# Kernel optimization log

Measured on AMD Instinct MI355X. Metric: run time of the kernel, lower is better.

Reference implementation:

```python
import jax, jax.numpy as jnp
import numpy as np

B, S = 1024, 256
E, EU = 8, 1            # total experts, universal experts
ES = E - EU             # specialized experts
UW = 0.3                # universal_expert_weight
NSTEPS = 1001
COV = 512
H = 128
DATA_DIM = 2


def setup_inputs() -> dict:
    key = jax.random.key(0)
    ks = iter(jax.random.split(key, 64))

    def nrm(shape, s=0.02):
        return jax.random.normal(next(ks), shape, jnp.float32) * s

    inp = {
        "y_t": jax.random.normal(next(ks), (B, S, 1), jnp.float32),
        "y_0_hat": jax.random.normal(next(ks), (B, S, 1), jnp.float32),
        "cov_embedding": jax.random.normal(next(ks), (B, COV), jnp.float32),
        "t": jax.random.randint(next(ks), (B,), 0, NSTEPS),
    }
    for l, nin in zip((1, 2, 3), (DATA_DIM, H, H)):
        inp[f"l{l}_emb"] = jax.random.uniform(next(ks), (NSTEPS, H), jnp.float32)  # embed.weight.uniform_()
        inp[f"l{l}_W"] = nrm((E, nin, H))      # per-expert Linear weights
        inp[f"l{l}_b"] = jnp.zeros((E, H), jnp.float32)
        inp[f"l{l}_Wc"] = nrm((COV, H))        # cov_projection
        inp[f"l{l}_bc"] = jnp.zeros((H,), jnp.float32)
        inp[f"l{l}_Wr1"] = nrm((COV, COV // 2))  # specialized_router layer 1
        inp[f"l{l}_br1"] = jnp.zeros((COV // 2,), jnp.float32)
        inp[f"l{l}_Wr2"] = nrm((COV // 2, ES))   # specialized_router layer 2
        inp[f"l{l}_br2"] = jnp.zeros((ES,), jnp.float32)
    inp["W4"] = nrm((H, 1))
    inp["b4"] = jnp.zeros((1,), jnp.float32)
    return inp


def _moe_layer(x, t, cov, emb, W, b, Wc, bc, Wr1, br1, Wr2, br2):
    # x: [B,S,in]; t: [B] int; cov: [B,COV]
    gamma = emb[t][:, None, :]                                   # [B,1,H]
    hr = jax.nn.relu(cov @ Wr1 + br1)                            # router (dropout inactive in eval)
    rw = jax.nn.softmax(hr @ Wr2 + br2, axis=-1) * (1.0 - UW)    # [B,ES] specialized routing weights
    w = jnp.concatenate(
        [jnp.full((x.shape[0], EU), UW / EU, x.dtype), rw], axis=1
    )                                                            # [B,E] full routing weights
    # gamma factors out of the weighted sum over experts, so fuse expert GEMMs + weighting:
    mix = jnp.einsum('bsi,eio,be->bso', x, W, w) + jnp.einsum('be,eo->bo', w, b)[:, None, :]
    mix = gamma * mix
    cov_gamma = cov @ Wc + bc                                    # [B,H]
    mix = mix * (1.0 + cov_gamma[:, None, :])
    usage = rw.mean(axis=0)                                      # mean over batch
    load = jnp.mean((usage - 1.0 / ES) ** 2)                     # mse vs uniform
    return mix, load


def reference(y_t, y_0_hat, cov_embedding, t,
              l1_emb, l1_W, l1_b, l1_Wc, l1_bc, l1_Wr1, l1_br1, l1_Wr2, l1_br2,
              l2_emb, l2_W, l2_b, l2_Wc, l2_bc, l2_Wr1, l2_br1, l2_Wr2, l2_br2,
              l3_emb, l3_W, l3_b, l3_Wc, l3_bc, l3_Wr1, l3_br1, l3_Wr2, l3_br2,
              W4, b4):
    h = jnp.concatenate([y_t, y_0_hat], axis=-1)                 # cat_y_pred: [B,S,2]
    h, ld1 = _moe_layer(h, t, cov_embedding, l1_emb, l1_W, l1_b, l1_Wc, l1_bc, l1_Wr1, l1_br1, l1_Wr2, l1_br2)
    h = jax.nn.softplus(h)
    h, ld2 = _moe_layer(h, t, cov_embedding, l2_emb, l2_W, l2_b, l2_Wc, l2_bc, l2_Wr1, l2_br1, l2_Wr2, l2_br2)
    h = jax.nn.softplus(h)
    h, ld3 = _moe_layer(h, t, cov_embedding, l3_emb, l3_W, l3_b, l3_Wc, l3_bc, l3_Wr1, l3_br1, l3_Wr2, l3_br2)
    h = jax.nn.softplus(h)
    out = h @ W4 + b4                                            # [B,S,1] velocity
    return out, ld1 + ld2 + ld3
```

## Files before the change

### kernel.cpp

```cpp
#include <hip/hip_runtime.h>
#include <hip/hip_bf16.h>
#include <math.h>

#define B_    1024
#define S_    256
#define COV_  512
#define H_    128
#define E_    8
#define ES_   7

#define W_WS_OFF   0
#define COVG_OFF   24576
#define USAGE_OFF  417792

#define AT_STRIDE  136
#define WT_STRIDE  40

typedef __attribute__((ext_vector_type(8))) short bf16x8;
typedef __attribute__((ext_vector_type(4))) float f32x4;

__device__ __forceinline__ float softplus_f(float x) {
    return fmaxf(x, 0.0f) + __logf(1.0f + __expf(-fabsf(x)));
}

__device__ __forceinline__ unsigned pk2_bf16(float a, float b) {
    __hip_bfloat162 h = __float22bfloat162_rn(make_float2(a, b));
    return *reinterpret_cast<unsigned*>(&h);
}
__device__ __forceinline__ void split_pair(float a, float b, unsigned &hi, unsigned &lo) {
    hi = pk2_bf16(a, b);
    float ha = __uint_as_float(hi << 16);
    float hb = __uint_as_float(hi & 0xffff0000u);
    lo = pk2_bf16(a - ha, b - hb);
}

struct RouterArgs {
    const float* cov;
    const float* Wr1[3];
    const float* br1[3];
    const float* Wr2[3];
    const float* br2[3];
    const float* Wc[3];
    const float* bc[3];
    float* ws;
};

__global__ __launch_bounds__(384) void router_kernel(RouterArgs a) {
    const int l   = blockIdx.y;
    const int b0  = blockIdx.x * 4;
    const int tid = threadIdx.x;

    __shared__ float hr[4][256];
    __shared__ float susage[ES_];
    if (tid < ES_) susage[tid] = 0.0f;

    const float* __restrict__ c0 = a.cov + (size_t)(b0 + 0) * COV_;
    const float* __restrict__ c1 = a.cov + (size_t)(b0 + 1) * COV_;
    const float* __restrict__ c2 = a.cov + (size_t)(b0 + 2) * COV_;
    const float* __restrict__ c3 = a.cov + (size_t)(b0 + 3) * COV_;

    {
        const float* __restrict__ Wp;
        int stride; float bias;
        if (tid < 256) { Wp = a.Wr1[l] + tid;         stride = 256; bias = a.br1[l][tid]; }
        else           { Wp = a.Wc[l]  + (tid - 256); stride = 128; bias = a.bc[l][tid - 256]; }

        float acc0 = 0.f, acc1 = 0.f, acc2 = 0.f, acc3 = 0.f;
        #pragma unroll 8
        for (int k = 0; k < COV_; ++k) {
            const float wv = Wp[(size_t)k * stride];
            acc0 = fmaf(c0[k], wv, acc0);
            acc1 = fmaf(c1[k], wv, acc1);
            acc2 = fmaf(c2[k], wv, acc2);
            acc3 = fmaf(c3[k], wv, acc3);
        }
        if (tid < 256) {
            hr[0][tid] = fmaxf(acc0 + bias, 0.0f);
            hr[1][tid] = fmaxf(acc1 + bias, 0.0f);
            hr[2][tid] = fmaxf(acc2 + bias, 0.0f);
            hr[3][tid] = fmaxf(acc3 + bias, 0.0f);
        } else {
            const int j = tid - 256;
            a.ws[COVG_OFF + (size_t)(l * B_ + b0 + 0) * H_ + j] = acc0 + bias;
            a.ws[COVG_OFF + (size_t)(l * B_ + b0 + 1) * H_ + j] = acc1 + bias;
            a.ws[COVG_OFF + (size_t)(l * B_ + b0 + 2) * H_ + j] = acc2 + bias;
            a.ws[COVG_OFF + (size_t)(l * B_ + b0 + 3) * H_ + j] = acc3 + bias;
        }
    }
    __syncthreads();

    {
        const int wave = tid >> 6;
        const int lane = tid & 63;
        if (wave < 4) {
            const int bb = wave;
            const int o = lane >> 3;
            const int g = lane & 7;
            float p = 0.0f;
            if (o < ES_) {
                #pragma unroll
                for (int m = 0; m < 32; ++m) {
                    const int k = g * 32 + m;
                    p = fmaf(hr[bb][k], a.Wr2[l][k * ES_ + o], p);
                }
            }
            p += __shfl_xor(p, 1);
            p += __shfl_xor(p, 2);
            p += __shfl_xor(p, 4);
            const float lg = p + ((o < ES_) ? a.br2[l][o] : 0.0f);
            float v[ES_];
            #pragma unroll
            for (int oo = 0; oo < ES_; ++oo) v[oo] = __shfl(lg, oo * 8, 64);
            if (lane == 0) {
                const int b = b0 + bb;
                float mx = v[0];
                #pragma unroll
                for (int oo = 1; oo < ES_; ++oo) mx = fmaxf(mx, v[oo]);
                float ex[ES_]; float s = 0.0f;
                #pragma unroll
                for (int oo = 0; oo < ES_; ++oo) { ex[oo] = __expf(v[oo] - mx); s += ex[oo]; }
                const float inv = 0.7f / s;
                float* wout = a.ws + W_WS_OFF + (size_t)(l * B_ + b) * 8;
                wout[0] = 0.3f;
                #pragma unroll
                for (int oo = 0; oo < ES_; ++oo) {
                    const float rwv = ex[oo] * inv;
                    wout[1 + oo] = rwv;
                    atomicAdd(&susage[oo], rwv);
                }
            }
        }
    }
    __syncthreads();
    if (tid < ES_) atomicAdd(a.ws + USAGE_OFF + l * ES_ + tid, susage[tid]);
}

struct MainArgs {
    const float* y_t;
    const float* y0;
    const int*   t;
    const float* emb[3];
    const float* W1;
    const float* W2;
    const float* W3;
    const float* b_[3];
    const float* W4;
    const float* b4;
    float* ws;
    float* out;
};

__global__ __launch_bounds__(1024, 4) void main_kernel(MainArgs a) {
    __shared__ unsigned short Ahi[256 * AT_STRIDE];
    __shared__ unsigned short Alo[256 * AT_STRIDE];
    __shared__ unsigned short WtBuf[2][128 * WT_STRIDE];
    __shared__ float GPs[2][128];
    __shared__ float GPBs[2][128];
    __shared__ float W4s[128];

    const int tid  = threadIdx.x;
    const int b    = blockIdx.x;
    const int lane = tid & 63;
    const int w    = tid >> 6;
    const int wm   = w >> 1;
    const int wn   = w & 1;
    const int nl   = lane & 15;
    const int quad = lane >> 4;
    const int tb   = a.t[b];

    float* L1f = (float*)WtBuf;

    if (tid < 384) {
        const int l = tid >> 7, j = tid & 127;
        const float* wv = a.ws + W_WS_OFF + (size_t)(l * B_ + b) * 8;
        const float gamma = a.emb[l][tb * H_ + j];
        const float covg  = a.ws[COVG_OFF + (size_t)(l * B_ + b) * H_ + j];
        const float gp = gamma * (1.0f + covg);
        const float* bl = a.b_[l];
        float bm = 0.0f;
        #pragma unroll
        for (int e = 0; e < E_; ++e) bm = fmaf(wv[e], bl[e * H_ + j], bm);
        if (l == 0) {
            float s0 = 0.0f, s1 = 0.0f;
            #pragma unroll
            for (int e = 0; e < E_; ++e) {
                s0 = fmaf(wv[e], a.W1[e * 256 + j], s0);
                s1 = fmaf(wv[e], a.W1[e * 256 + 128 + j], s1);
            }
            L1f[j]       = gp * s0;
            L1f[128 + j] = gp * s1;
            L1f[256 + j] = gp * bm;
        } else {
            GPs[l - 1][j]  = gp;
            GPBs[l - 1][j] = gp * bm;
        }
    }
    if (tid < 128) W4s[tid] = a.W4[tid];
    __syncthreads();

    {
        const int tok = tid >> 2;
        const int jh  = (tid & 3) * 32;
        const float x0 = a.y_t[b * S_ + tok];
        const float x1 = a.y0[b * S_ + tok];
        #pragma unroll
        for (int g = 0; g < 4; ++g) {
            const int jb = jh + g * 8;
            unsigned hp[4], lp[4];
            #pragma unroll
            for (int p = 0; p < 4; ++p) {
                const int j0 = jb + 2 * p;
                float m0 = fmaf(x0, L1f[j0],     fmaf(x1, L1f[128 + j0],     L1f[256 + j0]));
                float m1 = fmaf(x0, L1f[j0 + 1], fmaf(x1, L1f[128 + j0 + 1], L1f[256 + j0 + 1]));
                split_pair(softplus_f(m0), softplus_f(m1), hp[p], lp[p]);
            }
            *(uint4*)&Ahi[tok * AT_STRIDE + jb] = make_uint4(hp[0], hp[1], hp[2], hp[3]);
            *(uint4*)&Alo[tok * AT_STRIDE + jb] = make_uint4(lp[0], lp[1], lp[2], lp[3]);
        }
    }

    const int bj  = tid & 127;
    const int bkg = tid >> 7;

    for (int L = 0; L < 2; ++L) {
        const float* __restrict__ Wg = L ? a.W3 : a.W2;
        const float* wv = a.ws + W_WS_OFF + (size_t)((L + 1) * B_ + b) * 8;
        float we[E_];
        #pragma unroll
        for (int e = 0; e < E_; ++e) we[e] = wv[e];

        f32x4 acc[2][4];
        #pragma unroll
        for (int mt = 0; mt < 2; ++mt)
            #pragma unroll
            for (int nt = 0; nt < 4; ++nt)
                acc[mt][nt] = (f32x4){0.f, 0.f, 0.f, 0.f};

        unsigned bh[2], blo_[2];
        auto build = [&](int kc) {
            float bacc[4] = {0.f, 0.f, 0.f, 0.f};
            const float* base = Wg + (size_t)(kc * 32 + bkg * 4) * H_ + bj;
            #pragma unroll
            for (int e = 0; e < E_; ++e) {
                const float* p = base + (size_t)e * (H_ * H_);
                const float wE = we[e];
                #pragma unroll
                for (int i = 0; i < 4; ++i)
                    bacc[i] = fmaf(wE, p[i * H_], bacc[i]);
            }
            split_pair(bacc[0], bacc[1], bh[0], blo_[0]);
            split_pair(bacc[2], bacc[3], bh[1], blo_[1]);
        };

        build(0);

        for (int kc = 0; kc < 4; ++kc) {
            __syncthreads();
            *(uint2*)&WtBuf[0][bj * WT_STRIDE + bkg * 4] = make_uint2(bh[0], bh[1]);
            *(uint2*)&WtBuf[1][bj * WT_STRIDE + bkg * 4] = make_uint2(blo_[0], blo_[1]);
            __syncthreads();

            const int ka = kc * 32 + quad * 8;
            bf16x8 Af[2], Al[2], Bf[4], Bl[4];
            #pragma unroll
            for (int mt = 0; mt < 2; ++mt) {
                const int row = (wm * 32 + mt * 16 + nl) * AT_STRIDE + ka;
                Af[mt] = *(const bf16x8*)&Ahi[row];
                Al[mt] = *(const bf16x8*)&Alo[row];
            }
            #pragma unroll
            for (int nt = 0; nt < 4; ++nt) {
                const int row = (wn * 64 + nt * 16 + nl) * WT_STRIDE + quad * 8;
                Bf[nt] = *(const bf16x8*)&WtBuf[0][row];
                Bl[nt] = *(const bf16x8*)&WtBuf[1][row];
            }
            #pragma unroll
            for (int mt = 0; mt < 2; ++mt)
                #pragma unroll
                for (int nt = 0; nt < 4; ++nt) {
                    acc[mt][nt] = __builtin_amdgcn_mfma_f32_16x16x32_bf16(Af[mt], Bf[nt], acc[mt][nt], 0, 0, 0);
                    acc[mt][nt] = __builtin_amdgcn_mfma_f32_16x16x32_bf16(Af[mt], Bl[nt], acc[mt][nt], 0, 0, 0);
                    acc[mt][nt] = __builtin_amdgcn_mfma_f32_16x16x32_bf16(Al[mt], Bf[nt], acc[mt][nt], 0, 0, 0);
                }

            if (kc < 3) build(kc + 1);
        }
        __syncthreads();

        if (L == 0) {
            #pragma unroll
            for (int nt = 0; nt < 4; ++nt) {
                const int n = wn * 64 + nt * 16 + nl;
                const float gp = GPs[0][n], gpb = GPBs[0][n];
                #pragma unroll
                for (int mt = 0; mt < 2; ++mt) {
                    const int tok0 = wm * 32 + mt * 16 + quad * 4;
                    #pragma unroll
                    for (int rp = 0; rp < 2; ++rp) {
                        const float h0 = softplus_f(fmaf(gp, acc[mt][nt][2 * rp],     gpb));
                        const float h1 = softplus_f(fmaf(gp, acc[mt][nt][2 * rp + 1], gpb));
                        unsigned hh, ll;
                        split_pair(h0, h1, hh, ll);
                        const int t0 = tok0 + 2 * rp;
                        Ahi[t0 * AT_STRIDE + n]       = (unsigned short)hh;
                        Ahi[(t0 + 1) * AT_STRIDE + n] = (unsigned short)(hh >> 16);
                        Alo[t0 * AT_STRIDE + n]       = (unsigned short)ll;
                        Alo[(t0 + 1) * AT_STRIDE + n] = (unsigned short)(ll >> 16);
                    }
                }
            }
        } else {
            float po[2][4];
            #pragma unroll
            for (int mt = 0; mt < 2; ++mt)
                #pragma unroll
                for (int r = 0; r < 4; ++r) po[mt][r] = 0.0f;
            #pragma unroll
            for (int nt = 0; nt < 4; ++nt) {
                const int n = wn * 64 + nt * 16 + nl;
                const float gp = GPs[1][n], gpb = GPBs[1][n], w4 = W4s[n];
                #pragma unroll
                for (int mt = 0; mt < 2; ++mt)
                    #pragma unroll
                    for (int r = 0; r < 4; ++r) {
                        const float h = softplus_f(fmaf(gp, acc[mt][nt][r], gpb));
                        po[mt][r] = fmaf(h, w4, po[mt][r]);
                    }
            }
            #pragma unroll
            for (int mt = 0; mt < 2; ++mt)
                #pragma unroll
                for (int r = 0; r < 4; ++r) {
                    po[mt][r] += __shfl_xor(po[mt][r], 1);
                    po[mt][r] += __shfl_xor(po[mt][r], 2);
                    po[mt][r] += __shfl_xor(po[mt][r], 4);
                    po[mt][r] += __shfl_xor(po[mt][r], 8);
                }
            float* pos = (float*)WtBuf;
            if (nl == 0) {
                #pragma unroll
                for (int mt = 0; mt < 2; ++mt)
                    #pragma unroll
                    for (int r = 0; r < 4; ++r)
                        pos[(wm * 32 + mt * 16 + quad * 4 + r) * 2 + wn] = po[mt][r];
            }
            __syncthreads();
            if (tid < 256)
                a.out[b * S_ + tid] = pos[2 * tid] + pos[2 * tid + 1] + a.b4[0];
        }
    }

    if (b == 0 && tid == 0) {
        float ld = 0.0f;
        for (int l = 0; l < 3; ++l)
            for (int o = 0; o < ES_; ++o) {
                float u = a.ws[USAGE_OFF + l * ES_ + o] * (1.0f / (float)B_);
                float d = u - (1.0f / (float)ES_);
                ld = fmaf(d, d, ld);
            }
        a.out[B_ * S_] = ld * (1.0f / (float)ES_);
    }
}

extern "C" void kernel_launch(void* const* d_in, const int* in_sizes, int n_in,
                              void* d_out, int out_size, void* d_ws, size_t ws_size,
                              hipStream_t stream) {
    (void)in_sizes; (void)n_in; (void)out_size; (void)ws_size;

    RouterArgs ra;
    ra.cov = (const float*)d_in[2];
    ra.ws  = (float*)d_ws;

    MainArgs ma;
    ma.y_t = (const float*)d_in[0];
    ma.y0  = (const float*)d_in[1];
    ma.t   = (const int*)d_in[3];
    for (int l = 0; l < 3; ++l) {
        const int base = 4 + l * 9;
        ma.emb[l] = (const float*)d_in[base + 0];
        ma.b_[l]  = (const float*)d_in[base + 2];
        ra.Wc[l]  = (const float*)d_in[base + 3];
        ra.bc[l]  = (const float*)d_in[base + 4];
        ra.Wr1[l] = (const float*)d_in[base + 5];
        ra.br1[l] = (const float*)d_in[base + 6];
        ra.Wr2[l] = (const float*)d_in[base + 7];
        ra.br2[l] = (const float*)d_in[base + 8];
    }
    ma.W1 = (const float*)d_in[4 + 0 * 9 + 1];
    ma.W2 = (const float*)d_in[4 + 1 * 9 + 1];
    ma.W3 = (const float*)d_in[4 + 2 * 9 + 1];
    ma.W4 = (const float*)d_in[31];
    ma.b4 = (const float*)d_in[32];
    ma.ws  = (float*)d_ws;
    ma.out = (float*)d_out;

    (void)hipMemsetAsync((char*)d_ws + USAGE_OFF * sizeof(float), 0, 24 * sizeof(float), stream);
    router_kernel<<<dim3(256, 3, 1), 384, 0, stream>>>(ra);
    main_kernel<<<dim3(1024, 1, 1), 1024, 0, stream>>>(ma);
}
```

Baseline: 287.7 us.

## Restructure router GEMM with LDS-staged cov, 8-row blocking and split-K

The router kernel now handles 8 batch rows per block instead of 4 and stages the cov rows in shared memory as float4. Each thread computes two output columns for all 8 rows over a quarter of K, using float2 weight loads. A shared-memory reduction then combines the four K slices. The aim is to double weight reuse per load and cut redundant global cov reads. The cost is about 60KB of LDS per block, more registers and an extra sync pass, with only half as many blocks.

```diff
diff --git a/kernel.cpp b/kernel.cpp
--- a/kernel.cpp
+++ b/kernel.cpp
@@ -45,46 +45,80 @@
     float* ws;
 };
 
-__global__ __launch_bounds__(384) void router_kernel(RouterArgs a) {
+__global__ __launch_bounds__(768) void router_kernel(RouterArgs a) {
     const int l   = blockIdx.y;
-    const int b0  = blockIdx.x * 4;
+    const int b0  = blockIdx.x * 8;
     const int tid = threadIdx.x;
 
-    __shared__ float hr[4][256];
-    __shared__ float susage[ES_];
+    __shared__ float4 covs[8][COV_ / 4];
+    __shared__ float  part[4][3072];
+    __shared__ float  hr[8][256];
+    __shared__ float  susage[ES_];
     if (tid < ES_) susage[tid] = 0.0f;
 
-    const float* __restrict__ c0 = a.cov + (size_t)(b0 + 0) * COV_;
-    const float* __restrict__ c1 = a.cov + (size_t)(b0 + 1) * COV_;
-    const float* __restrict__ c2 = a.cov + (size_t)(b0 + 2) * COV_;
-    const float* __restrict__ c3 = a.cov + (size_t)(b0 + 3) * COV_;
+    for (int f = tid; f < 1024; f += 768) {
+        const int bb = f >> 7, k4 = f & 127;
+        covs[bb][k4] = ((const float4*)(a.cov + (size_t)(b0 + bb) * COV_))[k4];
+    }
+    __syncthreads();
 
     {
-        const float* __restrict__ Wp;
-        int stride; float bias;
-        if (tid < 256) { Wp = a.Wr1[l] + tid;         stride = 256; bias = a.br1[l][tid]; }
-        else           { Wp = a.Wc[l]  + (tid - 256); stride = 128; bias = a.bc[l][tid - 256]; }
-
-        float acc0 = 0.f, acc1 = 0.f, acc2 = 0.f, acc3 = 0.f;
-        #pragma unroll 8
-        for (int k = 0; k < COV_; ++k) {
-            const float wv = Wp[(size_t)k * stride];
-            acc0 = fmaf(c0[k], wv, acc0);
-            acc1 = fmaf(c1[k], wv, acc1);
-            acc2 = fmaf(c2[k], wv, acc2);
-            acc3 = fmaf(c3[k], wv, acc3);
-        }
-        if (tid < 256) {
-            hr[0][tid] = fmaxf(acc0 + bias, 0.0f);
-            hr[1][tid] = fmaxf(acc1 + bias, 0.0f);
-            hr[2][tid] = fmaxf(acc2 + bias, 0.0f);
-            hr[3][tid] = fmaxf(acc3 + bias, 0.0f);
+        const int cp = tid % 192;
+        const int ks = tid / 192;
+        const int c0 = cp * 2;
+        const float* __restrict__ Wp; int rs;
+        if (c0 < 256) { Wp = a.Wr1[l] + c0;         rs = 256; }
+        else          { Wp = a.Wc[l]  + (c0 - 256); rs = 128; }
+
+        float acc0[8], acc1[8];
+        #pragma unroll
+        for (int bb = 0; bb < 8; ++bb) { acc0[bb] = 0.f; acc1[bb] = 0.f; }
+
+        const int k4beg = ks * 32, k4end = k4beg + 32;
+        #pragma unroll 2
+        for (int k4 = k4beg; k4 < k4end; ++k4) {
+            float2 w0 = *(const float2*)(Wp + (size_t)(4 * k4 + 0) * rs);
+            float2 w1 = *(const float2*)(Wp + (size_t)(4 * k4 + 1) * rs);
+            float2 w2 = *(const float2*)(Wp + (size_t)(4 * k4 + 2) * rs);
+            float2 w3 = *(const float2*)(Wp + (size_t)(4 * k4 + 3) * rs);
+            #pragma unroll
+            for (int bb = 0; bb < 8; ++bb) {
+                float4 cv = covs[bb][k4];
+                acc0[bb] = fmaf(cv.x, w0.x, acc0[bb]);
+                acc1[bb] = fmaf(cv.x, w0.y, acc1[bb]);
+                acc0[bb] = fmaf(cv.y, w1.x, acc0[bb]);
+                acc1[bb] = fmaf(cv.y, w1.y, acc1[bb]);
+                acc0[bb] = fmaf(cv.z, w2.x, acc0[bb]);
+                acc1[bb] = fmaf(cv.z, w2.y, acc1[bb]);
+                acc0[bb] = fmaf(cv.w, w3.x, acc0[bb]);
+                acc1[bb] = fmaf(cv.w, w3.y, acc1[bb]);
+            }
+        }
+        #pragma unroll
+        for (int bb = 0; bb < 8; ++bb)
+            *(float2*)&part[ks][bb * 384 + c0] = make_float2(acc0[bb], acc1[bb]);
+    }
+    __syncthreads();
+
+    {
+        const int p0 = tid * 4;
+        float4 s = {0.f, 0.f, 0.f, 0.f};
+        #pragma unroll
+        for (int ks = 0; ks < 4; ++ks) {
+            float4 v = *(const float4*)&part[ks][p0];
+            s.x += v.x; s.y += v.y; s.z += v.z; s.w += v.w;
+        }
+        const int bb = p0 / 384;
+        const int c  = p0 % 384;
+        const float sv[4] = {s.x, s.y, s.z, s.w};
+        if (c < 256) {
+            #pragma unroll
+            for (int q = 0; q < 4; ++q)
+                hr[bb][c + q] = fmaxf(sv[q] + a.br1[l][c + q], 0.0f);
         } else {
-            const int j = tid - 256;
-            a.ws[COVG_OFF + (size_t)(l * B_ + b0 + 0) * H_ + j] = acc0 + bias;
-            a.ws[COVG_OFF + (size_t)(l * B_ + b0 + 1) * H_ + j] = acc1 + bias;
-            a.ws[COVG_OFF + (size_t)(l * B_ + b0 + 2) * H_ + j] = acc2 + bias;
-            a.ws[COVG_OFF + (size_t)(l * B_ + b0 + 3) * H_ + j] = acc3 + bias;
+            #pragma unroll
+            for (int q = 0; q < 4; ++q)
+                a.ws[COVG_OFF + (size_t)(l * B_ + b0 + bb) * H_ + (c - 256 + q)] = sv[q] + a.bc[l][c - 256 + q];
         }
     }
     __syncthreads();
@@ -92,7 +126,7 @@
     {
         const int wave = tid >> 6;
         const int lane = tid & 63;
-        if (wave < 4) {
+        if (wave < 8) {
             const int bb = wave;
             const int o = lane >> 3;
             const int g = lane & 7;
@@ -395,6 +429,6 @@
     ma.out = (float*)d_out;
 
     (void)hipMemsetAsync((char*)d_ws + USAGE_OFF * sizeof(float), 0, 24 * sizeof(float), stream);
-    router_kernel<<<dim3(256, 3, 1), 384, 0, stream>>>(ra);
+    router_kernel<<<dim3(128, 3, 1), 768, 0, stream>>>(ra);
     main_kernel<<<dim3(1024, 1, 1), 1024, 0, stream>>>(ma);
 }
```

Measured after the change: 291.4 us. About the same (+1.3%).
